# Optimization experiments

Hardware: AMD Instinct MI355X
Metric: run time of the kernel (lower is better)

## Reference

```python
import jax, jax.numpy as jnp
import numpy as np

# dims
B, H, W = 2, 128, 256
MD = 34            # model_dim (last 2 channels = sin/cos lat)
LD = MD - 2        # learnable_dim = 32
NH, HD = 4, 8      # n_heads, head_dim
SH = 64            # shared_hidden (DISCO out channels)
K = 25             # number of DISCO basis functions (5x5 kernel_shape)
P = 7              # local stencil width (lat x lon support of geodesic basis)
R = P // 2
FF1, FF2 = 512, 256


def setup_inputs() -> dict:
    key = jax.random.key(0)
    ks = jax.random.split(key, 16)
    x = jax.random.normal(ks[0], (B, H, W, MD), dtype=jnp.float32)
    # latitude-dependent sparse geodesic basis values over a 7x7 stencil
    psi_val = jax.random.uniform(ks[1], (K, H, P * P), dtype=jnp.float32) * 0.1
    disco_w = jax.random.normal(ks[2], (SH, K), dtype=jnp.float32) * 0.1
    disco_b = jax.random.normal(ks[3], (SH,), dtype=jnp.float32) * 0.01
    # per-head MLP: shared_hidden -> 32 -> 1
    hw1 = jax.random.normal(ks[4], (NH, SH, 32), dtype=jnp.float32) * (1.0 / np.sqrt(SH))
    hb1 = jax.random.normal(ks[5], (NH, 32), dtype=jnp.float32) * 0.01
    hw2 = jax.random.normal(ks[6], (NH, 32, 1), dtype=jnp.float32) * (1.0 / np.sqrt(32))
    hb2 = jax.random.normal(ks[7], (NH, 1), dtype=jnp.float32) * 0.01
    # FFN: model_dim -> 512 -> 256 -> learnable_dim
    fw1 = jax.random.normal(ks[8], (MD, FF1), dtype=jnp.float32) * (1.0 / np.sqrt(MD))
    fw1 = fw1.at[-2:, :].set(0.0)  # matches ffn[0].weight[:, -2:] = 0 init
    fb1 = jax.random.normal(ks[9], (FF1,), dtype=jnp.float32) * 0.01
    fw2 = jax.random.normal(ks[10], (FF1, FF2), dtype=jnp.float32) * (1.0 / np.sqrt(FF1))
    fb2 = jax.random.normal(ks[11], (FF2,), dtype=jnp.float32) * 0.01
    fw3 = jax.random.normal(ks[12], (FF2, LD), dtype=jnp.float32) * (1.0 / np.sqrt(FF2))
    fb3 = jax.random.normal(ks[13], (LD,), dtype=jnp.float32) * 0.01
    return {"x": x, "psi_val": psi_val, "disco_w": disco_w, "disco_b": disco_b,
            "hw1": hw1, "hb1": hb1, "hw2": hw2, "hb2": hb2,
            "fw1": fw1, "fb1": fb1, "fw2": fw2, "fb2": fb2, "fw3": fw3, "fb3": fb3}


def _gelu(t):
    return jax.nn.gelu(t, approximate=False)  # torch nn.GELU default (erf)


def _disco_s2(xn, psi_val, disco_w, disco_b):
    """DISCO sparse-basis conv on single-channel maps.
    xn: (N, H, W). Basis values vary with output latitude, longitude is
    translation-invariant; support is a lat-clamped / lon-wrapped 7x7 stencil.
    Returns (N, SH, H, W)."""
    xp = jnp.pad(xn, ((0, 0), (R, R), (0, 0)), mode="edge")  # clamp at poles
    shifts = []
    for dlat in range(P):
        row = xp[:, dlat:dlat + H, :]
        for dlon in range(-R, R + 1):
            shifts.append(jnp.roll(row, -dlon, axis=2))  # wrap in longitude
    xs = jnp.stack(shifts, axis=1)  # (N, P*P, H, W)
    basis = jnp.einsum("khp,nphw->nkhw", psi_val, xs)       # basis aggregation
    return jnp.einsum("fk,nkhw->nfhw", disco_w, basis) + disco_b[None, :, None, None]


def reference(x, psi_val, disco_w, disco_b, hw1, hb1, hw2, hb2,
              fw1, fb1, fw2, fb2, fw3, fb3):
    x_learn = x[..., :LD]
    sin_cos = x[..., LD:]
    x_res = x_learn
    # (B,H,W,LD) -> (B*LD, H, W): each learnable channel is a 1-channel map
    xn = x_learn.transpose(0, 3, 1, 2).reshape(B * LD, H, W)
    d = _disco_s2(xn, psi_val, disco_w, disco_b)              # (B*LD, SH, H, W)
    d = d.reshape(B, LD, SH, H, W).transpose(0, 3, 4, 1, 2)    # (B,H,W,LD,SH)
    # per-head MLP over its head_dim slice (head index is outer in LD)
    d = d.reshape(B, H, W, NH, HD, SH)
    h = _gelu(jnp.einsum("bxynds,nso->bxyndo", d, hw1) + hb1[None, None, None, :, None, :])
    h = jnp.einsum("bxyndo,noe->bxynde", h, hw2) + hb2[None, None, None, :, None, :]
    x_learn = h[..., 0].reshape(B, H, W, LD)
    x_learn = x_learn + x_res                                  # use_residual
    x_full = jnp.concatenate([x_learn, sin_cos], axis=-1)
    x_res2 = x_learn
    t = _gelu(x_full @ fw1 + fb1)
    t = _gelu(t @ fw2 + fb2)
    t = t @ fw3 + fb3                                          # dropout p=0 -> id
    x_learn = t + x_res2
    return jnp.concatenate([x_learn, sin_cos], axis=-1)
```

## Files before the change

kernel.cpp:

```cpp
#include <hip/hip_runtime.h>
#include <math.h>


typedef __attribute__((ext_vector_type(8))) short bfrag;
typedef __attribute__((ext_vector_type(4))) float ffrag;
typedef __attribute__((ext_vector_type(4))) short short4v;

union bfi4 { int4 i; bfrag b; };

__device__ __forceinline__ float gelu_f(float v) {
  const float z = v * (2.3022077484f + 0.1029451564f * v * v);
  const float e = __builtin_amdgcn_exp2f(-z);
  return v * __builtin_amdgcn_rcpf(1.0f + e);
}

__device__ __forceinline__ short f2bf(float f) {
  union { float f; unsigned u; } v; v.f = f;
  unsigned r = (v.u + 0x7fffu + ((v.u >> 16) & 1u)) >> 16;
  return (short)r;
}

__device__ __forceinline__ short f2bf_fast(float f) {
  union { float f; unsigned u; } v; v.f = f;
  return (short)((v.u + 0x8000u) >> 16);
}

__device__ __forceinline__ float bf2f(short s) {
  union { float f; unsigned u; } v;
  v.u = ((unsigned)(unsigned short)s) << 16;
  return v.f;
}

template <int CTRL>
__device__ __forceinline__ float dpp_add(float v) {
  union { float f; int i; } s, t;
  s.f = v;
  t.i = __builtin_amdgcn_update_dpp(0, s.i, CTRL, 0xf, 0xf, true);
  return v + t.f;
}
__device__ __forceinline__ float reduce16(float v) {
  v = dpp_add<0xB1>(v);
  v = dpp_add<0x4E>(v);
  v = dpp_add<0x141>(v);
  v = dpp_add<0x140>(v);
  return v;
}

__device__ __forceinline__ void st4bf(short* p, float4 v) {
  short4v s;
  s[0] = f2bf(v.x); s[1] = f2bf(v.y); s[2] = f2bf(v.z); s[3] = f2bf(v.w);
  *(short4v*)p = s;
}

__global__ __launch_bounds__(256) void k01_prep(
    const float* __restrict__ psi, const float* __restrict__ dw,
    const float* __restrict__ db,
    const float* __restrict__ fw1, const float* __restrict__ fw2,
    const float* __restrict__ fw3, const float* __restrict__ hw1,
    const float* __restrict__ hb1,
    short* __restrict__ wcb, short* __restrict__ fw1s,
    short* __restrict__ fw2s, short* __restrict__ fw3s,
    float* __restrict__ hb1e) {
  __shared__ __align__(16) char sm[59392];
  const int bid = blockIdx.x;
  const int tid = threadIdx.x;

  if (bid < 128) {
    float* tileL = (float*)sm;
    short* tile2 = (short*)(sm + 13312);
    float* hw1L  = (float*)(sm + 26624);
    const int h = bid;
    const int lane = tid & 63;
    const int w = __builtin_amdgcn_readfirstlane(tid >> 6);

    for (int e = tid; e < 2048; e += 256)
      ((float4*)hw1L)[e] = ((const float4*)hw1)[e];

    float dwreg[25];
#pragma unroll
    for (int kk = 0; kk < 25; ++kk) dwreg[kk] = dw[lane * 25 + kk];
    const int p0 = w * 13;
    const int pend = (p0 + 13 < 49) ? (p0 + 13) : 49;
#pragma unroll 1
    for (int p = p0; p < pend; ++p) {
      float acc = 0.f;
#pragma unroll
      for (int kk = 0; kk < 25; ++kk)
        acc += dwreg[kk] * psi[kk * 6272 + h * 49 + p];
      tileL[lane * 52 + p] = acc;
    }
    __syncthreads();

    for (int e = tid; e < 4096; e += 256) {
      const int no = e >> 5, pp = e & 31;
      if (pp < 25) {
        const int p2 = pp * 2;
        const int nn = no >> 5, o = no & 31;
        const float* hp = hw1L + nn * 2048 + o;
        float a0 = 0.f, a1 = 0.f;
#pragma unroll 4
        for (int f = 0; f < 64; ++f) {
          const float wv = hp[f * 32];
          a0 += wv * tileL[f * 52 + p2];
          a1 += wv * tileL[f * 52 + p2 + 1];
        }
        tile2[no * 52 + p2] = f2bf(a0);
        if (p2 + 1 < 49) tile2[no * 52 + p2 + 1] = f2bf(a1);
      }
    }
    __syncthreads();

    short* outp = wcb + h * 16384;
    for (int idx = tid; idx < 16384; idx += 256) {
      const int jj = idx & 7, ln = (idx >> 3) & 63;
      const int nt = (idx >> 9) & 1, kt = (idx >> 10) & 1;
      const int par = (idx >> 11) & 1, nn = idx >> 12;
      const int k = kt * 32 + ((ln >> 4) << 3) + jj;
      const int o = nt * 16 + (ln & 15);
      const int r = k >> 3, dlt = k & 7;
      const int j = par ? (dlt - 1) : dlt;
      short v = 0;
      if (r < 7 && j >= 0 && j < 7) v = tile2[(nn * 32 + o) * 52 + r * 7 + j];
      outp[idx] = v;
    }
    return;
  }

  if (bid < 144) {
    short* S = (short*)sm;
    const int kt = bid - 128;
    const float* src = fw2 + kt * 8192;
    for (int q = tid; q < 2048; q += 256) {
      const int lin = q * 4;
      const int kk = lin >> 8, nn = lin & 255;
      st4bf(S + kk * 260 + nn, *(const float4*)(src + lin));
    }
    __syncthreads();
    short* dst = fw2s + kt * 8192;
    for (int q = tid; q < 8192; q += 256) {
      const int jj = q & 7, lane = (q >> 3) & 63, nt = q >> 9;
      const int kk = (lane >> 4) * 8 + jj, nn = nt * 16 + (lane & 15);
      dst[q] = S[kk * 260 + nn];
    }
    return;
  }

  if (bid == 144) {
    short* S = (short*)sm;
    for (int q = tid; q < 4096; q += 256) {
      const int lin = q * 4;
      const int kk = lin >> 9, nn = lin & 511;
      st4bf(S + kk * 516 + nn, *(const float4*)(fw1 + lin));
    }
    __syncthreads();
    for (int q = tid; q < 16384; q += 256) {
      const int jj = q & 7, lane = (q >> 3) & 63, nt = q >> 9;
      const int kk = (lane >> 4) * 8 + jj, nn = nt * 16 + (lane & 15);
      fw1s[q] = S[kk * 516 + nn];
    }
    return;
  }

  if (bid == 145) {
    short* S = (short*)sm;
    for (int q = tid; q < 2048; q += 256) {
      const int lin = q * 4;
      const int kk = lin >> 5, nn = lin & 31;
      st4bf(S + kk * 36 + nn, *(const float4*)(fw3 + lin));
    }
    __syncthreads();
    for (int q = tid; q < 8192; q += 256) {
      const int jj = q & 7, lane = (q >> 3) & 63;
      const int nt = (q >> 9) & 1, kt = q >> 10;
      const int kk = kt * 32 + (lane >> 4) * 8 + jj, nn = nt * 16 + (lane & 15);
      fw3s[q] = S[kk * 36 + nn];
    }
    return;
  }

  if (tid < 128) {
    const int n = tid >> 5, o = tid & 31;
    float acc = hb1[n * 32 + o];
#pragma unroll
    for (int s = 0; s < 64; ++s)
      acc += hw1[n * 2048 + s * 32 + o] * db[s];
    hb1e[tid] = acc;
  }
}

__global__ __launch_bounds__(256, 6) void k23_fused(
    const float* __restrict__ x,    const short* __restrict__ wcb,
    const float* __restrict__ hb1e, const float* __restrict__ hw2,
    const float* __restrict__ hb2,
    const short* __restrict__ fw1s, const short* __restrict__ fw2s,
    const short* __restrict__ fw3s,
    const float* __restrict__ fb1,  const float* __restrict__ fb2,
    const float* __restrict__ fb3,  float* __restrict__ outb) {
  __shared__ __align__(16) char smem[27008];
  short* sX = (short*)smem;
  short* sM = (short*)(smem + 24832);

  const int tid = threadIdx.x;
  const int w0  = blockIdx.x * 32;
  const int h   = blockIdx.y;
  const int b   = blockIdx.z;

  {
    int4* p = (int4*)sX;
    int4 z; z.x = z.y = z.z = z.w = 0;
    for (int e = tid; e < (32 * 388) / 8; e += 256) p[e] = z;
  }
  __syncthreads();

#pragma unroll 1
  for (int r = 0; r < 7; ++r) {
    int hr = h - 3 + r; hr = hr < 0 ? 0 : (hr > 127 ? 127 : hr);
    const float* __restrict__ xrow = x + (size_t)((b * 128 + hr) * 256) * 34;
    short* __restrict__ sxr = sX + r * 48;
    for (int e = tid; e < 39 * 16; e += 256) {
      const int c2 = e & 15;
      const int wp = e >> 4;
      const int wr = (w0 - 3 + wp) & 255;
      const float2 v = *(const float2*)&xrow[wr * 34 + c2 * 2];
      short* dp = sxr + (c2 * 2) * 388 + wp;
      dp[0]   = f2bf_fast(v.x);
      dp[388] = f2bf_fast(v.y);
    }
  }

  if (tid < 64) {
    const int wl = tid >> 1;
    const int sc = tid & 1;
    const int idx = ((b * 128 + h) * 256 + (w0 + wl)) * 34 + 32 + sc;
    outb[idx] = x[idx];
  }
  __syncthreads();

  const int lane = tid & 63, lm = lane & 15, lq = lane >> 4;
  const int n = tid >> 6;

  float hb1v[2], hw2v[2];
#pragma unroll
  for (int nt = 0; nt < 2; ++nt) {
    hb1v[nt] = hb1e[n * 32 + nt * 16 + lm];
    hw2v[nt] = hw2[n * 32 + nt * 16 + lm];
  }
  const float hb2n = hb2[n];

  bfrag cW[2][2][2];
#pragma unroll
  for (int par = 0; par < 2; ++par)
#pragma unroll
    for (int kt = 0; kt < 2; ++kt)
#pragma unroll
      for (int nt = 0; nt < 2; ++nt)
        cW[par][kt][nt] = *(const bfrag*)(wcb + h * 16384 + n * 4096 +
                            ((par * 2 + kt) * 2 + nt) * 512 + lane * 8);

  const int* tpB = (const int*)sX;

#pragma unroll 1
  for (int i = 0; i < 8; ++i) {
    const int c = n * 8 + i;

    const int base0 = c * 194 + lq * 24 + lm;
    bfi4 u0, u1;
    u0.i.x = tpB[base0];      u0.i.y = tpB[base0 + 1];
    u0.i.z = tpB[base0 + 2];  u0.i.w = tpB[base0 + 3];
    u1.i.x = tpB[base0 + 96]; u1.i.y = tpB[base0 + 97];
    u1.i.z = tpB[base0 + 98]; u1.i.w = tpB[base0 + 99];

#pragma unroll
    for (int par = 0; par < 2; ++par) {
      ffrag h0 = {0.f, 0.f, 0.f, 0.f}, h1 = {0.f, 0.f, 0.f, 0.f};
      h0 = __builtin_amdgcn_mfma_f32_16x16x32_bf16(u0.b, cW[par][0][0], h0, 0, 0, 0);
      h0 = __builtin_amdgcn_mfma_f32_16x16x32_bf16(u1.b, cW[par][1][0], h0, 0, 0, 0);
      h1 = __builtin_amdgcn_mfma_f32_16x16x32_bf16(u0.b, cW[par][0][1], h1, 0, 0, 0);
      h1 = __builtin_amdgcn_mfma_f32_16x16x32_bf16(u1.b, cW[par][1][1], h1, 0, 0, 0);

#pragma unroll
      for (int rr = 0; rr < 4; ++rr) {
        float v = gelu_f(h0[rr] + hb1v[0]) * hw2v[0] +
                  gelu_f(h1[rr] + hb1v[1]) * hw2v[1];
        v = reduce16(v);
        const int p = 2 * (lq * 4 + rr) + par;
        const float res = bf2f(sX[c * 388 + 144 + 3 + p]);
        if (lm == 0) sM[p * 34 + c] = f2bf_fast(v + hb2n + res);
      }
    }
  }
  __syncthreads();

  short* sT1h = (short*)smem;
  short* sT2  = (short*)smem;
  const int wave = n;
  const int koff = lq * 8;
  const int mt3 = wave & 1;
  const int nt3 = wave >> 1;
  const int col3 = nt3 * 16 + lm;
  const int pixg = (b * 128 + h) * 256 + w0;

  bfrag aF[2];
#pragma unroll
  for (int mt = 0; mt < 2; ++mt)
    aF[mt] = *(const bfrag*)(sM + (mt * 16 + lm) * 34 + koff);
  float res3[4];
#pragma unroll
  for (int r = 0; r < 4; ++r)
    res3[r] = bf2f(sM[(mt3 * 16 + lq * 4 + r) * 34 + col3]);

  const int n0 = wave * 4;
  ffrag acc[2][4];
#pragma unroll
  for (int mt = 0; mt < 2; ++mt)
#pragma unroll
    for (int ni = 0; ni < 4; ++ni) acc[mt][ni] = ffrag{0.f, 0.f, 0.f, 0.f};
  const short* w2base = fw2s + n0 * 512 + lane * 8;

#pragma unroll 1
  for (int H = 0; H < 2; ++H) {
    bfrag b1f[4];
#pragma unroll
    for (int ni = 0; ni < 4; ++ni)
      b1f[ni] = *(const bfrag*)(fw1s + (H * 16 + wave * 4 + ni) * 512 + lane * 8);
#pragma unroll
    for (int ni = 0; ni < 4; ++ni) {
      const int ntl = wave * 4 + ni;
#pragma unroll
      for (int mt = 0; mt < 2; ++mt) {
        ffrag cc = {0.f, 0.f, 0.f, 0.f};
        cc = __builtin_amdgcn_mfma_f32_16x16x32_bf16(aF[mt], b1f[ni], cc, 0, 0, 0);
        const int colg = H * 256 + ntl * 16 + lm;
        const float bias = fb1[colg];
#pragma unroll
        for (int r = 0; r < 4; ++r) {
          const int row = mt * 16 + lq * 4 + r;
          sT1h[row * 264 + ntl * 16 + lm] = f2bf_fast(gelu_f(cc[r] + bias));
        }
      }
    }
    __syncthreads();

#pragma unroll 2
    for (int kt = 0; kt < 8; ++kt) {
      bfrag bv[4];
#pragma unroll
      for (int ni = 0; ni < 4; ++ni)
        bv[ni] = *(const bfrag*)(w2base + (H * 8 + kt) * 8192 + ni * 512);
      const bfrag a0 = *(const bfrag*)(sT1h + lm * 264 + kt * 32 + koff);
      const bfrag a1 = *(const bfrag*)(sT1h + (16 + lm) * 264 + kt * 32 + koff);
#pragma unroll
      for (int ni = 0; ni < 4; ++ni) {
        acc[0][ni] = __builtin_amdgcn_mfma_f32_16x16x32_bf16(a0, bv[ni], acc[0][ni], 0, 0, 0);
        acc[1][ni] = __builtin_amdgcn_mfma_f32_16x16x32_bf16(a1, bv[ni], acc[1][ni], 0, 0, 0);
      }
    }
    __syncthreads();
  }

#pragma unroll
  for (int mt = 0; mt < 2; ++mt)
#pragma unroll
    for (int ni = 0; ni < 4; ++ni) {
      const int col = (n0 + ni) * 16 + lm;
      const float bias = fb2[col];
#pragma unroll
      for (int r = 0; r < 4; ++r) {
        const int row = mt * 16 + lq * 4 + r;
        sT2[row * 264 + col] = f2bf_fast(gelu_f(acc[mt][ni][r] + bias));
      }
    }
  __syncthreads();

  ffrag c3 = {0.f, 0.f, 0.f, 0.f};
  const short* sA3 = sT2 + (mt3 * 16 + lm) * 264 + koff;
#pragma unroll
  for (int kt = 0; kt < 8; ++kt) {
    const bfrag a = *(const bfrag*)(sA3 + kt * 32);
    const bfrag bw = *(const bfrag*)(fw3s + nt3 * 512 + kt * 1024 + lane * 8);
    c3 = __builtin_amdgcn_mfma_f32_16x16x32_bf16(a, bw, c3, 0, 0, 0);
  }
  {
    const float bias = fb3[col3];
#pragma unroll
    for (int r = 0; r < 4; ++r) {
      const int row = mt3 * 16 + lq * 4 + r;
      outb[(pixg + row) * 34 + col3] = c3[r] + bias + res3[r];
    }
  }
}

extern "C" void kernel_launch(void* const* d_in, const int* in_sizes, int n_in,
                              void* d_out, int out_size, void* d_ws, size_t ws_size,
                              hipStream_t stream) {
  const float* x   = (const float*)d_in[0];
  const float* psi = (const float*)d_in[1];
  const float* dw  = (const float*)d_in[2];
  const float* db  = (const float*)d_in[3];
  const float* hw1 = (const float*)d_in[4];
  const float* hb1 = (const float*)d_in[5];
  const float* hw2 = (const float*)d_in[6];
  const float* hb2 = (const float*)d_in[7];
  const float* fw1 = (const float*)d_in[8];
  const float* fb1 = (const float*)d_in[9];
  const float* fw2 = (const float*)d_in[10];
  const float* fb2 = (const float*)d_in[11];
  const float* fw3 = (const float*)d_in[12];
  const float* fb3 = (const float*)d_in[13];
  float* outb = (float*)d_out;

  short* wcb  = (short*)d_ws;
  short* fw1s = wcb + 2097152;
  short* fw2s = fw1s + 16384;
  short* fw3s = fw2s + 131072;
  float* hb1e = (float*)(fw3s + 8192);

  hipLaunchKernelGGL(k01_prep, dim3(147), dim3(256), 0, stream,
                     psi, dw, db, fw1, fw2, fw3, hw1, hb1,
                     wcb, fw1s, fw2s, fw3s, hb1e);
  hipLaunchKernelGGL(k23_fused, dim3(8, 128, 2), dim3(256), 0, stream,
                     x, wcb, hb1e, hw2, hb2,
                     fw1s, fw2s, fw3s, fb1, fb2, fb3, outb);
}
```

Baseline: 198.2 us.

## Split prep weight fold per head, remap blocks to XCDs, stage output stores

```diff
diff --git a/kernel.cpp b/kernel.cpp
--- a/kernel.cpp
+++ b/kernel.cpp
@@ -61,20 +61,21 @@
     short* __restrict__ wcb, short* __restrict__ fw1s,
     short* __restrict__ fw2s, short* __restrict__ fw3s,
     float* __restrict__ hb1e) {
-  __shared__ __align__(16) char sm[59392];
+  __shared__ __align__(16) char sm[33024];
   const int bid = blockIdx.x;
   const int tid = threadIdx.x;
 
-  if (bid < 128) {
+  if (bid < 512) {
     float* tileL = (float*)sm;
-    short* tile2 = (short*)(sm + 13312);
-    float* hw1L  = (float*)(sm + 26624);
-    const int h = bid;
+    float* hw1n  = (float*)(sm + 13312);
+    short* tile2 = (short*)(sm + 21504);
+    const int h = bid >> 2;
+    const int n = bid & 3;
     const int lane = tid & 63;
     const int w = __builtin_amdgcn_readfirstlane(tid >> 6);
 
-    for (int e = tid; e < 2048; e += 256)
-      ((float4*)hw1L)[e] = ((const float4*)hw1)[e];
+    for (int e = tid; e < 512; e += 256)
+      ((float4*)hw1n)[e] = ((const float4*)(hw1 + n * 2048))[e];
 
     float dwreg[25];
 #pragma unroll
@@ -91,44 +92,41 @@
     }
     __syncthreads();
 
-    for (int e = tid; e < 4096; e += 256) {
-      const int no = e >> 5, pp = e & 31;
-      if (pp < 25) {
-        const int p2 = pp * 2;
-        const int nn = no >> 5, o = no & 31;
-        const float* hp = hw1L + nn * 2048 + o;
-        float a0 = 0.f, a1 = 0.f;
+    const int o = tid & 31;
+#pragma unroll 1
+    for (int pp = tid >> 5; pp < 25; pp += 8) {
+      const int p2 = pp * 2;
+      float a0 = 0.f, a1 = 0.f;
 #pragma unroll 4
-        for (int f = 0; f < 64; ++f) {
-          const float wv = hp[f * 32];
-          a0 += wv * tileL[f * 52 + p2];
-          a1 += wv * tileL[f * 52 + p2 + 1];
-        }
-        tile2[no * 52 + p2] = f2bf(a0);
-        if (p2 + 1 < 49) tile2[no * 52 + p2 + 1] = f2bf(a1);
+      for (int f = 0; f < 64; ++f) {
+        const float wv = hw1n[f * 32 + o];
+        a0 += wv * tileL[f * 52 + p2];
+        a1 += wv * tileL[f * 52 + p2 + 1];
       }
-    }
-    __syncthreads();
-
-    short* outp = wcb + h * 16384;
-    for (int idx = tid; idx < 16384; idx += 256) {
+      tile2[o * 52 + p2] = f2bf(a0);
+      if (p2 + 1 < 49) tile2[o * 52 + p2 + 1] = f2bf(a1);
+    }
+    __syncthreads();
+
+    short* outp = wcb + h * 16384 + n * 4096;
+    for (int idx = tid; idx < 4096; idx += 256) {
       const int jj = idx & 7, ln = (idx >> 3) & 63;
       const int nt = (idx >> 9) & 1, kt = (idx >> 10) & 1;
-      const int par = (idx >> 11) & 1, nn = idx >> 12;
+      const int par = idx >> 11;
       const int k = kt * 32 + ((ln >> 4) << 3) + jj;
-      const int o = nt * 16 + (ln & 15);
+      const int oo = nt * 16 + (ln & 15);
       const int r = k >> 3, dlt = k & 7;
       const int j = par ? (dlt - 1) : dlt;
       short v = 0;
-      if (r < 7 && j >= 0 && j < 7) v = tile2[(nn * 32 + o) * 52 + r * 7 + j];
+      if (r < 7 && j >= 0 && j < 7) v = tile2[oo * 52 + r * 7 + j];
       outp[idx] = v;
     }
     return;
   }
 
-  if (bid < 144) {
+  if (bid < 528) {
     short* S = (short*)sm;
-    const int kt = bid - 128;
+    const int kt = bid - 512;
     const float* src = fw2 + kt * 8192;
     for (int q = tid; q < 2048; q += 256) {
       const int lin = q * 4;
@@ -145,7 +143,7 @@
     return;
   }
 
-  if (bid == 144) {
+  if (bid == 528) {
     short* S = (short*)sm;
     for (int q = tid; q < 4096; q += 256) {
       const int lin = q * 4;
@@ -161,7 +159,7 @@
     return;
   }
 
-  if (bid == 145) {
+  if (bid == 529) {
     short* S = (short*)sm;
     for (int q = tid; q < 2048; q += 256) {
       const int lin = q * 4;
@@ -199,11 +197,39 @@
   __shared__ __align__(16) char smem[27008];
   short* sX = (short*)smem;
   short* sM = (short*)(smem + 24832);
+  float* sO = (float*)(smem + 16896);
 
   const int tid = threadIdx.x;
-  const int w0  = blockIdx.x * 32;
-  const int h   = blockIdx.y;
-  const int b   = blockIdx.z;
+
+  const int lin  = blockIdx.x + (blockIdx.y << 3) + (blockIdx.z << 10);
+  const int xcd  = lin & 7;
+  const int slot = lin >> 3;
+  const int w0   = (slot & 7) * 32;
+  const int b    = (slot >> 3) & 1;
+  const int h    = (xcd << 4) | (slot >> 4);
+
+  const int lane = tid & 63, lm = lane & 15, lq = lane >> 4;
+  const int n = tid >> 6;
+
+  bfrag cW[2][2][2];
+#pragma unroll
+  for (int par = 0; par < 2; ++par)
+#pragma unroll
+    for (int kt = 0; kt < 2; ++kt)
+#pragma unroll
+      for (int nt = 0; nt < 2; ++nt)
+        cW[par][kt][nt] = *(const bfrag*)(wcb + h * 16384 + n * 4096 +
+                            ((par * 2 + kt) * 2 + nt) * 512 + lane * 8);
+  float2 scv;
+  if (tid < 32)
+    scv = *(const float2*)&x[(size_t)(((b * 128 + h) * 256 + w0 + tid)) * 34 + 32];
+  float hb1v[2], hw2v[2];
+#pragma unroll
+  for (int nt = 0; nt < 2; ++nt) {
+    hb1v[nt] = hb1e[n * 32 + nt * 16 + lm];
+    hw2v[nt] = hw2[n * 32 + nt * 16 + lm];
+  }
+  const float hb2n = hb2[n];
 
   {
     int4* p = (int4*)sX;
@@ -227,35 +253,7 @@
       dp[388] = f2bf_fast(v.y);
     }
   }
-
-  if (tid < 64) {
-    const int wl = tid >> 1;
-    const int sc = tid & 1;
-    const int idx = ((b * 128 + h) * 256 + (w0 + wl)) * 34 + 32 + sc;
-    outb[idx] = x[idx];
-  }
   __syncthreads();
-
-  const int lane = tid & 63, lm = lane & 15, lq = lane >> 4;
-  const int n = tid >> 6;
-
-  float hb1v[2], hw2v[2];
-#pragma unroll
-  for (int nt = 0; nt < 2; ++nt) {
-    hb1v[nt] = hb1e[n * 32 + nt * 16 + lm];
-    hw2v[nt] = hw2[n * 32 + nt * 16 + lm];
-  }
-  const float hb2n = hb2[n];
-
-  bfrag cW[2][2][2];
-#pragma unroll
-  for (int par = 0; par < 2; ++par)
-#pragma unroll
-    for (int kt = 0; kt < 2; ++kt)
-#pragma unroll
-      for (int nt = 0; nt < 2; ++nt)
-        cW[par][kt][nt] = *(const bfrag*)(wcb + h * 16384 + n * 4096 +
-                            ((par * 2 + kt) * 2 + nt) * 512 + lane * 8);
 
   const int* tpB = (const int*)sX;
 
@@ -385,8 +383,15 @@
 #pragma unroll
     for (int r = 0; r < 4; ++r) {
       const int row = mt3 * 16 + lq * 4 + r;
-      outb[(pixg + row) * 34 + col3] = c3[r] + bias + res3[r];
-    }
+      sO[row * 34 + col3] = c3[r] + bias + res3[r];
+    }
+  }
+  if (tid < 32) { sO[tid * 34 + 32] = scv.x; sO[tid * 34 + 33] = scv.y; }
+  __syncthreads();
+  {
+    const float4* sp = (const float4*)sO;
+    float4* dp = (float4*)(outb + (size_t)pixg * 34);
+    for (int e = tid; e < 272; e += 256) dp[e] = sp[e];
   }
 }
 
@@ -415,7 +420,7 @@
   short* fw3s = fw2s + 131072;
   float* hb1e = (float*)(fw3s + 8192);
 
-  hipLaunchKernelGGL(k01_prep, dim3(147), dim3(256), 0, stream,
+  hipLaunchKernelGGL(k01_prep, dim3(531), dim3(256), 0, stream,
                      psi, dw, db, fw1, fw2, fw3, hw1, hb1,
                      wcb, fw1s, fw2s, fw3s, hb1e);
   hipLaunchKernelGGL(k23_fused, dim3(8, 128, 2), dim3(256), 0, stream,
```

New measurement: 178.7 us. 9.8% less time.
